# Kernel tuning notes

Measured on AMD Instinct MI355X. Metric: run time of the kernel, lower is better.

Reference implementation:

```python
import jax, jax.numpy as jnp
import numpy as np

V, D, L = 256, 512, 12
B, S = 8, 8192
EPS = 1e-5


def layernorm(x, g, b):
    mu = jnp.mean(x, axis=-1, keepdims=True)
    var = jnp.var(x, axis=-1, keepdims=True)
    return (x - mu) * jax.lax.rsqrt(var + EPS) * g + b


def log_g(x):
    # log of g(x) = x+0.5 if x>=0 else sigmoid(x)
    return jnp.where(x >= 0, jnp.log(jax.nn.relu(x) + 0.5), -jax.nn.softplus(-x))


def heinsen_scan_log(log_coeffs, log_values):
    # h_t = a_t * h_{t-1} + b_t in log-space, parallel over seq (axis=1)
    a_star = jnp.cumsum(log_coeffs, axis=1)
    log_h0_plus_b = jax.lax.cumlogsumexp(log_values - a_star, axis=1)
    return jnp.exp(a_star + log_h0_plus_b)


def min_gru(x, W):
    hg = x @ W                      # [B,S,2D]
    hidden, gate = hg[..., :D], hg[..., D:]
    log_coeffs = -jax.nn.softplus(gate)      # log(1 - z)
    log_z = -jax.nn.softplus(-gate)          # log z
    log_values = log_z + log_g(hidden)
    return heinsen_scan_log(log_coeffs, log_values)


def setup_inputs() -> dict:
    key = jax.random.key(0)
    k0, k1, k2 = jax.random.split(key, 3)
    tokens = jax.random.randint(k0, (B, S), 0, V)
    emb = jax.random.normal(k1, (V, D), dtype=jnp.float32) * 0.02
    # xavier uniform for Linear(D, 2D): fan_in=D, fan_out=2D
    lim = float(np.sqrt(6.0 / (D + 2 * D)))
    W = jax.random.uniform(k2, (L, D, 2 * D), minval=-lim, maxval=lim, dtype=jnp.float32)
    return {
        "tokens": tokens,
        "emb": emb,
        "ln_g": jnp.ones((L, D), jnp.float32),
        "ln_b": jnp.zeros((L, D), jnp.float32),
        "W": W,
        "norm_g": jnp.ones((D,), jnp.float32),
        "norm_b": jnp.zeros((D,), jnp.float32),
    }


def reference(tokens, emb, ln_g, ln_b, W, norm_g, norm_b):
    x = emb[tokens]                 # [B,S,D]
    for i in range(L):
        h = layernorm(x, ln_g[i], ln_b[i])
        x = x + min_gru(h, W[i])
    x = layernorm(x, norm_g, norm_b)
    logits = x @ emb.T              # tied lm_head, [B,S,V]
    return logits
```

## Files before the change

kernel.cpp:

```cpp
#include <hip/hip_runtime.h>
#include <stdint.h>

#define D 512
#define VOCAB 256
#define NLAYER 12
#define BB 8
#define SS 8192
#define CH 128
#define SL 64

typedef __bf16 bf16x8 __attribute__((ext_vector_type(8)));
typedef float f32x4 __attribute__((ext_vector_type(4)));
typedef _Float16 half2_t __attribute__((ext_vector_type(2)));

__device__ __forceinline__ unsigned short f2bf(float f) {
  union { float f; uint32_t u; } c; c.f = f;
  uint32_t u = c.u;
  u += 0x7FFFu + ((u >> 16) & 1u);
  return (unsigned short)(u >> 16);
}

__device__ __forceinline__ float rcpf_(float x) { return __builtin_amdgcn_rcpf(x); }

__device__ __forceinline__ uint32_t pack_fv(float f, float v) {
  union { half2_t h; uint32_t u; } c;
  c.h.x = (_Float16)f;
  c.h.y = (_Float16)v;
  return c.u;
}

__device__ __forceinline__ void unpack_fv(uint32_t u, float& f, float& v) {
  union { uint32_t u; half2_t h; } c; c.u = u;
  f = (float)c.h.x;
  v = (float)c.h.y;
}

__device__ __forceinline__ void gl_lds16(const unsigned short* g, unsigned short* l) {
  __builtin_amdgcn_global_load_lds((const __attribute__((address_space(1))) void*)(const void*)g,
                                   (__attribute__((address_space(3))) void*)(void*)l, 16, 0, 0);
}

__global__ __launch_bounds__(256) void k_gather(const int* __restrict__ toks,
                                                const float* __restrict__ emb,
                                                const float* __restrict__ g,
                                                const float* __restrict__ b,
                                                float* __restrict__ x,
                                                unsigned short* __restrict__ o) {
  int T = blockIdx.x * 256 + threadIdx.x;
  int row = T >> 6, lane = T & 63;
  int tok = toks[row] & (VOCAB - 1);
  const float4* s = (const float4*)(emb + (size_t)tok * D) + lane * 2;
  float4 v0 = s[0], v1 = s[1];
  float4* d = (float4*)(x + (size_t)row * D) + lane * 2;
  d[0] = v0;
  d[1] = v1;
  float sm = v0.x + v0.y + v0.z + v0.w + v1.x + v1.y + v1.z + v1.w;
  float ss = v0.x * v0.x + v0.y * v0.y + v0.z * v0.z + v0.w * v0.w +
             v1.x * v1.x + v1.y * v1.y + v1.z * v1.z + v1.w * v1.w;
  for (int m = 32; m; m >>= 1) {
    sm += __shfl_xor(sm, m, 64);
    ss += __shfl_xor(ss, m, 64);
  }
  float mu = sm * (1.0f / 512.0f);
  float var = ss * (1.0f / 512.0f) - mu * mu;
  float rstd = rsqrtf(var + 1e-5f);
  const float4* gp = (const float4*)g + lane * 2;
  const float4* bp = (const float4*)b + lane * 2;
  float4 g0 = gp[0], g1 = gp[1], b0 = bp[0], b1 = bp[1];
  uint32_t w0 = (uint32_t)f2bf((v0.x - mu) * rstd * g0.x + b0.x) |
                ((uint32_t)f2bf((v0.y - mu) * rstd * g0.y + b0.y) << 16);
  uint32_t w1 = (uint32_t)f2bf((v0.z - mu) * rstd * g0.z + b0.z) |
                ((uint32_t)f2bf((v0.w - mu) * rstd * g0.w + b0.w) << 16);
  uint32_t w2 = (uint32_t)f2bf((v1.x - mu) * rstd * g1.x + b1.x) |
                ((uint32_t)f2bf((v1.y - mu) * rstd * g1.y + b1.y) << 16);
  uint32_t w3 = (uint32_t)f2bf((v1.z - mu) * rstd * g1.z + b1.z) |
                ((uint32_t)f2bf((v1.w - mu) * rstd * g1.w + b1.w) << 16);
  uint4 r; r.x = w0; r.y = w1; r.z = w2; r.w = w3;
  ((uint4*)(o + (size_t)row * D))[lane] = r;
}

__global__ __launch_bounds__(256) void k_convW(const float* __restrict__ W,
                                               unsigned short* __restrict__ Wt) {
  __shared__ float tile[32][33];
  int bid = blockIdx.x;
  int l = bid >> 9;
  int rem = bid & 511;
  int kt = rem >> 5, nt = rem & 31;
  int k0 = kt * 32, n0 = nt * 32;
  int tx = threadIdx.x & 31, ty = threadIdx.x >> 5;
  const float* Wl = W + (size_t)l * D * 2 * D;
  for (int i = 0; i < 4; i++) {
    int k = k0 + ty + 8 * i;
    tile[ty + 8 * i][tx] = Wl[(size_t)k * 1024 + n0 + tx];
  }
  __syncthreads();
  unsigned short* Wtl = Wt + (size_t)l * 1024 * D;
  for (int i = 0; i < 4; i++) {
    int n = n0 + ty + 8 * i;
    Wtl[(size_t)n * D + k0 + tx] = f2bf(tile[tx][ty + 8 * i]);
  }
}

__global__ __launch_bounds__(256) void k_fragW(const unsigned short* __restrict__ Wt,
                                               unsigned short* __restrict__ WtF) {
  int t = blockIdx.x * 256 + threadIdx.x;
  int lane = t & 63;
  int tile = t >> 6;
  int l = tile >> 10;
  int rem = tile & 1023;
  int n16 = rem >> 4, kt = rem & 15;
  const unsigned short* src = Wt + (size_t)l * 1024 * 512 +
                              (size_t)(n16 * 16 + (lane & 15)) * 512 + kt * 32 + (lane >> 4) * 8;
  *(uint4*)(WtF + (size_t)l * 524288 + ((size_t)rem * 64 + lane) * 8) = *(const uint4*)src;
}

__global__ __launch_bounds__(256) void k_convEmb(const float* __restrict__ e,
                                                 unsigned short* __restrict__ o) {
  int t = blockIdx.x * 256 + threadIdx.x;
  const float4* s = (const float4*)e + (size_t)t * 2;
  float4 a = s[0], b = s[1];
  uint32_t w0 = (uint32_t)f2bf(a.x) | ((uint32_t)f2bf(a.y) << 16);
  uint32_t w1 = (uint32_t)f2bf(a.z) | ((uint32_t)f2bf(a.w) << 16);
  uint32_t w2 = (uint32_t)f2bf(b.x) | ((uint32_t)f2bf(b.y) << 16);
  uint32_t w3 = (uint32_t)f2bf(b.z) | ((uint32_t)f2bf(b.w) << 16);
  uint4 r; r.x = w0; r.y = w1; r.z = w2; r.w = w3;
  ((uint4*)o)[t] = r;
}

__global__ __launch_bounds__(256, 2) void k_gemm_act(const unsigned short* __restrict__ A,
                                                     const unsigned short* __restrict__ Bt,
                                                     uint32_t* __restrict__ fv,
                                                     float* __restrict__ P,
                                                     float* __restrict__ Q) {
  __shared__ __align__(16) unsigned short As[64 * 512];
  const int tid = threadIdx.x;
  const int lane = tid & 63;
  const int wave = tid >> 6;
  const int m0 = blockIdx.x * 64;
  const int qm = lane & 15;
  const int hi = lane >> 4;
  for (int j = 0; j < 16; j++) {
    int r = wave * 16 + j;
    int cg = (lane & ~7) | ((lane & 7) ^ (r & 7));
    gl_lds16(A + (size_t)(m0 + r) * 512 + cg * 8, As + r * 512);
  }
  __syncthreads();

  const int b_loc = m0 >> 13;
  const int c_chunk = (m0 & (SS - 1)) >> 6;
  const size_t pq0 = ((size_t)b_loc * CH + c_chunk) * 512;

  for (int np = 0; np < 2; np++) {
    const int c0 = np * 256 + wave * 64;
    const int n16h = (c0 >> 4);
    f32x4 ah[4][4] = {};
    f32x4 ag[4][4] = {};
    bf16x8 bh[2][4], bg[2][4];
    for (int j = 0; j < 4; j++) {
      bh[0][j] = *(const bf16x8*)(Bt + (((size_t)(n16h + j) * 16 + 0) * 64 + lane) * 8);
      bg[0][j] = *(const bf16x8*)(Bt + (((size_t)(n16h + j + 32) * 16 + 0) * 64 + lane) * 8);
    }
    for (int kt = 0; kt < 16; kt++) {
      const int cur = kt & 1;
      if (kt < 15) {
        const int nxt = cur ^ 1;
        for (int j = 0; j < 4; j++) {
          bh[nxt][j] = *(const bf16x8*)(Bt + (((size_t)(n16h + j) * 16 + kt + 1) * 64 + lane) * 8);
          bg[nxt][j] = *(const bf16x8*)(Bt + (((size_t)(n16h + j + 32) * 16 + kt + 1) * 64 + lane) * 8);
        }
      }
      bf16x8 af[4];
      for (int i = 0; i < 4; i++) {
        int row = i * 16 + qm;
        int cgd = kt * 4 + hi;
        int cl = (cgd & ~7) | ((cgd & 7) ^ (row & 7));
        af[i] = *(const bf16x8*)(&As[row * 512 + cl * 8]);
      }
      for (int i = 0; i < 4; i++)
        for (int j = 0; j < 4; j++) {
          ah[i][j] = __builtin_amdgcn_mfma_f32_16x16x32_bf16(af[i], bh[cur][j], ah[i][j], 0, 0, 0);
          ag[i][j] = __builtin_amdgcn_mfma_f32_16x16x32_bf16(af[i], bg[cur][j], ag[i][j], 0, 0, 0);
        }
    }
    const int rq = hi * 4;
    for (int j = 0; j < 4; j++) {
      float cp = 1.f, cq = 0.f;
      for (int i = 0; i < 4; i++) {
        float sp = 1.f, sq = 0.f;
        for (int r = 0; r < 4; r++) {
          float h = ah[i][j][r];
          float g = ag[i][j][r];
          float e = __expf(g);
          float f = rcpf_(1.0f + e);
          float sg = 1.0f - f;
          float gf = h >= 0.0f ? h + 0.5f : rcpf_(1.0f + __expf(-h));
          float v = sg * gf;
          int rowg = m0 + i * 16 + rq + r;
          fv[(size_t)rowg * 512 + c0 + j * 16 + qm] = pack_fv(f, v);
          sp *= f;
          sq = sq * f + v;
        }
        float op = __shfl_xor(sp, 16), oq = __shfl_xor(sq, 16);
        float tp = sp * op;
        float tq = (lane & 16) ? (oq * sp + sq) : (sq * op + oq);
        op = __shfl_xor(tp, 32); oq = __shfl_xor(tq, 32);
        sp = tp * op;
        sq = (lane & 32) ? (oq * tp + tq) : (tq * op + oq);
        cq = cq * sp + sq;
        cp = cp * sp;
      }
      if (hi == 0) {
        P[pq0 + c0 + j * 16 + qm] = cp;
        Q[pq0 + c0 + j * 16 + qm] = cq;
      }
    }
  }
}

__global__ __launch_bounds__(256) void k_gemm(const unsigned short* __restrict__ A,
                                              const unsigned short* __restrict__ Bt,
                                              float* __restrict__ C, int N, int MT) {
  __shared__ __align__(16) unsigned short As[128 * 64];
  __shared__ __align__(16) unsigned short Bs[128 * 64];
  const int tid = threadIdx.x;
  const int lane = tid & 63;
  const int wave = tid >> 6;
  const int bid = blockIdx.x;
  const int mt = bid % MT;
  const int nt = bid / MT;
  const int m0 = mt * 128, n0 = nt * 128;
  const int wr = (wave >> 1) * 64;
  const int wc = (wave & 1) * 64;
  const int lrow = lane >> 3;
  const int lcs = ((lane & 7) ^ lrow) * 8;
  const unsigned short* Ag = A + (size_t)(m0 + wave * 32 + lrow) * 512 + lcs;
  const unsigned short* Bg = Bt + (size_t)(n0 + wave * 32 + lrow) * 512 + lcs;
  unsigned short* Al = As + wave * 32 * 64;
  unsigned short* Bl = Bs + wave * 32 * 64;
  const int qm = lane & 15;
  const int hi = lane >> 4;
  f32x4 acc[4][4] = {};
  for (int k0 = 0; k0 < 512; k0 += 64) {
    for (int j = 0; j < 4; j++) gl_lds16(Ag + k0 + (size_t)j * 8 * 512, Al + j * 512);
    for (int j = 0; j < 4; j++) gl_lds16(Bg + k0 + (size_t)j * 8 * 512, Bl + j * 512);
    __syncthreads();
    for (int ks = 0; ks < 2; ks++) {
      const int sw = ((ks * 4 + hi) ^ (qm & 7)) * 8;
      bf16x8 af[4], bfr[4];
      for (int i = 0; i < 4; i++) {
        af[i] = *(const bf16x8*)(&As[(wr + i * 16 + qm) * 64 + sw]);
        bfr[i] = *(const bf16x8*)(&Bs[(wc + i * 16 + qm) * 64 + sw]);
      }
      for (int i = 0; i < 4; i++)
        for (int j = 0; j < 4; j++)
          acc[i][j] = __builtin_amdgcn_mfma_f32_16x16x32_bf16(af[i], bfr[j], acc[i][j], 0, 0, 0);
    }
    __syncthreads();
  }
  const int col = lane & 15;
  const int rq = (lane >> 4) * 4;
  for (int i = 0; i < 4; i++)
    for (int j = 0; j < 4; j++)
      for (int r = 0; r < 4; r++)
        C[(size_t)(m0 + wr + i * 16 + rq + r) * N + (n0 + wc + j * 16 + col)] = acc[i][j][r];
}

__global__ __launch_bounds__(256) void k_scan2(const float* __restrict__ P,
                                               const float* __restrict__ Q,
                                               float* __restrict__ Hs) {
  int T = blockIdx.x * 256 + threadIdx.x;
  int d = T & 511;
  int b = T >> 9;
  float h = 0.f;
  for (int c = 0; c < CH; c++) {
    size_t i = ((size_t)b * CH + c) * 512 + d;
    Hs[i] = h;
    h = P[i] * h + Q[i];
  }
}

__global__ __launch_bounds__(512) void k_scan3(const uint32_t* __restrict__ fv,
                                               const float* __restrict__ Hs,
                                               float* __restrict__ x,
                                               const float* __restrict__ g,
                                               const float* __restrict__ b,
                                               unsigned short* __restrict__ o) {
  const int d = threadIdx.x;
  const int bc = blockIdx.x;
  const int c = bc & (CH - 1);
  const int bb = bc >> 7;
  const size_t row0 = ((size_t)bb * SS + (size_t)c * SL);
  const uint32_t* base = fv + row0 * 512 + d;
  float* xb = x + row0 * 512 + d;
  float h = Hs[(size_t)bc * 512 + d];
  for (int s = 0; s < SL; s++) {
    float f, v;
    unpack_fv(base[(size_t)s * 512], f, v);
    h = f * h + v;
    xb[(size_t)s * 512] += h;
  }
  __syncthreads();

  const int wv = threadIdx.x >> 6, lane = threadIdx.x & 63;
  const float4* gp = (const float4*)g + lane * 2;
  const float4* bp = (const float4*)b + lane * 2;
  float4 g0 = gp[0], g1 = gp[1], b0 = bp[0], b1 = bp[1];
  const float* xr0 = x + row0 * 512;
  for (int rr = 0; rr < 8; rr++) {
    int r = wv * 8 + rr;
    const float4* xr = (const float4*)(xr0 + (size_t)r * 512) + lane * 2;
    float4 v0 = xr[0], v1 = xr[1];
    float sm = v0.x + v0.y + v0.z + v0.w + v1.x + v1.y + v1.z + v1.w;
    float ss = v0.x * v0.x + v0.y * v0.y + v0.z * v0.z + v0.w * v0.w +
               v1.x * v1.x + v1.y * v1.y + v1.z * v1.z + v1.w * v1.w;
    for (int m = 32; m; m >>= 1) {
      sm += __shfl_xor(sm, m, 64);
      ss += __shfl_xor(ss, m, 64);
    }
    float mu = sm * (1.0f / 512.0f);
    float var = ss * (1.0f / 512.0f) - mu * mu;
    float rstd = rsqrtf(var + 1e-5f);
    uint32_t w0 = (uint32_t)f2bf((v0.x - mu) * rstd * g0.x + b0.x) |
                  ((uint32_t)f2bf((v0.y - mu) * rstd * g0.y + b0.y) << 16);
    uint32_t w1 = (uint32_t)f2bf((v0.z - mu) * rstd * g0.z + b0.z) |
                  ((uint32_t)f2bf((v0.w - mu) * rstd * g0.w + b0.w) << 16);
    uint32_t w2 = (uint32_t)f2bf((v1.x - mu) * rstd * g1.x + b1.x) |
                  ((uint32_t)f2bf((v1.y - mu) * rstd * g1.y + b1.y) << 16);
    uint32_t w3 = (uint32_t)f2bf((v1.z - mu) * rstd * g1.z + b1.z) |
                  ((uint32_t)f2bf((v1.w - mu) * rstd * g1.w + b1.w) << 16);
    uint4 rr4; rr4.x = w0; rr4.y = w1; rr4.z = w2; rr4.w = w3;
    ((uint4*)(o + (row0 + r) * 512))[lane] = rr4;
  }
}

extern "C" void kernel_launch(void* const* d_in, const int* in_sizes, int n_in,
                              void* d_out, int out_size, void* d_ws, size_t ws_size,
                              hipStream_t stream) {
  const int* toks = (const int*)d_in[0];
  const float* emb = (const float*)d_in[1];
  const float* ln_g = (const float*)d_in[2];
  const float* ln_b = (const float*)d_in[3];
  const float* W = (const float*)d_in[4];
  const float* norm_g = (const float*)d_in[5];
  const float* norm_b = (const float*)d_in[6];
  float* out = (float*)d_out;

  const int gbs[4] = {8, 4, 2, 1};
  int GB = 1;
  for (int i = 0; i < 4; i++) {
    size_t MGv = (size_t)gbs[i] * SS;
    size_t need = MGv * 5120 + 2 * 12582912 + 262144 + (size_t)gbs[i] * 786432;
    if (need <= ws_size) { GB = gbs[i]; break; }
  }
  const int MG = GB * SS;
  const int MT128 = MG / 128;

  char* p = (char*)d_ws;
  float* x = (float*)p;                     p += (size_t)MG * 2048;
  uint32_t* fv = (uint32_t*)p;              p += (size_t)MG * 2048;
  unsigned short* hbf = (unsigned short*)p; p += (size_t)MG * 1024;
  unsigned short* Wtrow = (unsigned short*)p; p += 12582912;
  unsigned short* WtF = (unsigned short*)p;   p += 12582912;
  unsigned short* ebf = (unsigned short*)p;   p += 262144;
  float* P = (float*)p;                     p += (size_t)GB * 262144;
  float* Q = (float*)p;                     p += (size_t)GB * 262144;
  float* Hs = (float*)p;

  k_convW<<<NLAYER * 512, 256, 0, stream>>>(W, Wtrow);
  k_fragW<<<NLAYER * 1024 * 64 / 256, 256, 0, stream>>>(Wtrow, WtF);
  k_convEmb<<<64, 256, 0, stream>>>(emb, ebf);

  for (int g = 0; g < BB / GB; g++) {
    const int* tg = toks + (size_t)g * MG;
    float* outg = out + (size_t)g * MG * VOCAB;

    k_gather<<<MG / 4, 256, 0, stream>>>(tg, emb, ln_g, ln_b, x, hbf);
    for (int l = 0; l < NLAYER; l++) {
      k_gemm_act<<<MG / 64, 256, 0, stream>>>(hbf, WtF + (size_t)l * 524288, fv, P, Q);
      k_scan2<<<GB * 2, 256, 0, stream>>>(P, Q, Hs);
      const float* gn = (l < NLAYER - 1) ? (ln_g + (size_t)(l + 1) * D) : norm_g;
      const float* bn = (l < NLAYER - 1) ? (ln_b + (size_t)(l + 1) * D) : norm_b;
      k_scan3<<<GB * CH, 512, 0, stream>>>(fv, Hs, x, gn, bn, hbf);
    }
    k_gemm<<<2 * MT128, 256, 0, stream>>>(hbf, ebf, outg, VOCAB, MT128);
  }
}
```

Measured before the change: 3.019 ms.

## Parallelize cross-chunk carry scan over chunk groups with two-level scan

The middle scan pass previously ran one thread per (batch, channel), serially walking all 128 chunk carries using only a few blocks. It now splits the chunks into 8 groups of 16 per warp, composes each group's affine (P,Q) transform, combines group prefixes through shared memory, and then replays each group to write the carries. This trades a second read of P and Q for far more parallelism and shorter serial chains in a latency-bound kernel.

```diff
diff --git a/kernel.cpp b/kernel.cpp
--- a/kernel.cpp
+++ b/kernel.cpp
@@ -265,18 +265,41 @@
         C[(size_t)(m0 + wr + i * 16 + rq + r) * N + (n0 + wc + j * 16 + col)] = acc[i][j][r];
 }
 
-__global__ __launch_bounds__(256) void k_scan2(const float* __restrict__ P,
+__global__ __launch_bounds__(512) void k_scan2(const float* __restrict__ P,
                                                const float* __restrict__ Q,
                                                float* __restrict__ Hs) {
-  int T = blockIdx.x * 256 + threadIdx.x;
-  int d = T & 511;
-  int b = T >> 9;
-  float h = 0.f;
-  for (int c = 0; c < CH; c++) {
-    size_t i = ((size_t)b * CH + c) * 512 + d;
+  __shared__ float lp[8][64];
+  __shared__ float lq[8][64];
+  const int lane = threadIdx.x & 63;
+  const int w = threadIdx.x >> 6;
+  const int dg = blockIdx.x & 7;
+  const int b = blockIdx.x >> 3;
+  const int d = dg * 64 + lane;
+  const int c0 = w * 16;
+  const size_t base = (size_t)b * CH * 512 + d;
+  float p = 1.f, q = 0.f;
+  for (int c = c0; c < c0 + 16; c++) {
+    size_t i = base + (size_t)c * 512;
+    float Pc = P[i], Qc = Q[i];
+    q = q * Pc + Qc;
+    p = p * Pc;
+  }
+  lp[w][lane] = p;
+  lq[w][lane] = q;
+  __syncthreads();
+  float qq = 0.f, pp = 1.f;
+  for (int ww = 0; ww < w; ww++) {
+    float a = lp[ww][lane], bq = lq[ww][lane];
+    qq = qq * a + bq;
+    pp = pp * a;
+  }
+  float h = qq;
+  for (int c = c0; c < c0 + 16; c++) {
+    size_t i = base + (size_t)c * 512;
     Hs[i] = h;
     h = P[i] * h + Q[i];
   }
+  (void)pp;
 }
 
 __global__ __launch_bounds__(512) void k_scan3(const uint32_t* __restrict__ fv,
@@ -377,7 +400,7 @@
     k_gather<<<MG / 4, 256, 0, stream>>>(tg, emb, ln_g, ln_b, x, hbf);
     for (int l = 0; l < NLAYER; l++) {
       k_gemm_act<<<MG / 64, 256, 0, stream>>>(hbf, WtF + (size_t)l * 524288, fv, P, Q);
-      k_scan2<<<GB * 2, 256, 0, stream>>>(P, Q, Hs);
+      k_scan2<<<GB * 8, 512, 0, stream>>>(P, Q, Hs);
       const float* gn = (l < NLAYER - 1) ? (ln_g + (size_t)(l + 1) * D) : norm_g;
       const float* bn = (l < NLAYER - 1) ? (ln_b + (size_t)(l + 1) * D) : norm_b;
       k_scan3<<<GB * CH, 512, 0, stream>>>(fv, Hs, x, gn, bn, hbf);
```

Measured after the change: 2.894 ms. 1.04x faster.
